# Optimization experiments

Measured on AMD Instinct MI355X. Metric: run time of the kernel, lower is better.

## Reference

```python
import jax, jax.numpy as jnp
import numpy as np

T, B, S, D = 128, 32, 100, 256  # targetL, batch, sourceL, output_size
EPS = 1e-6

def setup_inputs() -> dict:
    key = jax.random.key(0)
    ks = jax.random.split(key, 9)
    sc = 0.05  # weight init scale
    inp = {
        'prev_layer': jax.random.normal(ks[0], (T, B, D), dtype=jnp.float32),
        'hidden': jax.random.normal(ks[1], (B, D), dtype=jnp.float32),
        'enc_output': jax.random.normal(ks[2], (T * B, S, D), dtype=jnp.float32),
        # linear weights (layer_norm=True -> no biases on linears)
        'W_in': jax.random.normal(ks[3], (D, 3 * D), dtype=jnp.float32) * sc,
        'W_hid': jax.random.normal(ks[4], (D, D), dtype=jnp.float32) * sc,
        'W_ctx': jax.random.normal(ks[5], (D, D), dtype=jnp.float32) * sc,
        'W_enc': jax.random.normal(ks[6], (D, D), dtype=jnp.float32) * sc,
        'W_q': jax.random.normal(ks[7], (D, D), dtype=jnp.float32) * sc,   # MLPAttention query proj
        'v_att': jax.random.normal(ks[8], (D,), dtype=jnp.float32) * sc,  # MLPAttention score vector
        # layernorm affine params
        'g_pre': jnp.ones(3 * D, jnp.float32), 'b_pre': jnp.zeros(3 * D, jnp.float32),
        'g_enc': jnp.ones(D, jnp.float32), 'b_enc': jnp.zeros(D, jnp.float32),
        'g_h': jnp.ones(D, jnp.float32), 'b_h': jnp.zeros(D, jnp.float32),
        'g_c': jnp.ones(D, jnp.float32), 'b_c': jnp.zeros(D, jnp.float32),
        'g_q': jnp.ones(D, jnp.float32), 'b_q': jnp.zeros(D, jnp.float32),
    }
    return inp

def _ln(x, g, b):
    m = jnp.mean(x, axis=-1, keepdims=True)
    v = jnp.mean((x - m) ** 2, axis=-1, keepdims=True)
    return g * (x - m) / jnp.sqrt(v + EPS) + b

def reference(prev_layer, hidden, enc_output, W_in, W_hid, W_ctx, W_enc, W_q, v_att,
              g_pre, b_pre, g_enc, b_enc, g_h, b_h, g_c, b_c, g_q, b_q):
    Tl, Bb, Dd = prev_layer.shape
    # input / encoder projections (dropout=0 -> identity)
    preact = _ln(prev_layer @ W_in, g_pre, b_pre)        # [T,B,3D]
    pctx = _ln(enc_output @ W_enc, g_enc, b_enc)         # [T*B,S,D]
    z, h_gate, x_t = jnp.split(preact, 3, axis=-1)
    z = jax.nn.sigmoid(z)
    h_gate = jax.nn.sigmoid(h_gate)
    # SRU-style elementwise linear recurrence over time
    def step(h, zx):
        zt, xt = zx
        s = (1.0 - zt) * h + zt * xt
        return s, s
    final_h, ss = jax.lax.scan(step, hidden, (z, x_t))   # ss: [T,B,D]
    # MLP (Bahdanau) attention: scores = v . tanh(LN(Wq s) + pctx)
    q = _ln(ss @ W_q, g_q, b_q).reshape(Tl * Bb, 1, Dd)
    scores = jnp.einsum('nsd,d->ns', jnp.tanh(q + pctx), v_att)  # [T*B,S]
    attn = jax.nn.softmax(scores, axis=-1)
    attn_out = jnp.einsum('ns,nsd->nd', attn, pctx).reshape(Tl, Bb, Dd)
    attn_out = attn_out / np.sqrt(Dd).astype(np.float32)
    out = jnp.tanh(_ln(ss @ W_hid, g_h, b_h) + _ln(attn_out @ W_ctx, g_c, b_c))
    out = (1.0 - h_gate) * out + h_gate * prev_layer     # highway gate
    return out, final_h, attn
```

## Files before the change

### kernel.cpp

```cpp
#include <hip/hip_runtime.h>
#include <hip/hip_bf16.h>
#include <math.h>

typedef short  s16x8 __attribute__((ext_vector_type(8)));
typedef float  f32x4 __attribute__((ext_vector_type(4)));
typedef float  f32x2 __attribute__((ext_vector_type(2)));

#define LN_EPS 1e-6f

__device__ __forceinline__ unsigned short f2bf(float x) {
  union { float f; unsigned u; } v; v.f = x;
  unsigned r = v.u + 0x7FFFu + ((v.u >> 16) & 1u);
  return (unsigned short)(r >> 16);
}
__device__ __forceinline__ float bf2f(unsigned short u) {
  union { unsigned u; float f; } v; v.u = ((unsigned)u) << 16;
  return v.f;
}
__device__ __forceinline__ float bflo(unsigned u) {
  union { unsigned u; float f; } v; v.u = u << 16; return v.f;
}
__device__ __forceinline__ float bfhi(unsigned u) {
  union { unsigned u; float f; } v; v.u = u & 0xFFFF0000u; return v.f;
}
__device__ __forceinline__ unsigned pack_bf2(float a, float b) {
  __hip_bfloat162 h = __float22bfloat162_rn(make_float2(a, b));
  unsigned u; __builtin_memcpy(&u, &h, 4); return u;
}
__device__ __forceinline__ float fast_tanh(float x) {
  float e = __expf(2.0f * x);
  return 1.0f - 2.0f * __builtin_amdgcn_rcpf(e + 1.0f);
}
__device__ __forceinline__ float fast_sigmoid(float x) {
  return __builtin_amdgcn_rcpf(1.0f + __expf(-x));
}

template <int CTRL>
__device__ __forceinline__ float dpp_add(float v) {
  union { float f; int i; } a, r;
  a.f = v;
  r.i = __builtin_amdgcn_update_dpp(0, a.i, CTRL, 0xF, 0xF, true);
  return v + r.f;
}
template <int CTRL>
__device__ __forceinline__ float dpp_max(float v) {
  union { float f; int i; } a, r;
  a.f = v;
  r.i = __builtin_amdgcn_update_dpp(a.i, a.i, CTRL, 0xF, 0xF, false);
  return fmaxf(v, r.f);
}
__device__ __forceinline__ float bcast63(float v) {
  union { float f; int i; } a, r;
  a.f = v;
  r.i = __builtin_amdgcn_readlane(a.i, 63);
  return r.f;
}
__device__ __forceinline__ float wredsum(float v) {
  v = dpp_add<0x128>(v); v = dpp_add<0x124>(v); v = dpp_add<0x122>(v); v = dpp_add<0x121>(v);
  v = dpp_add<0x142>(v); v = dpp_add<0x143>(v);
  return bcast63(v);
}
__device__ __forceinline__ float wredmax(float v) {
  v = dpp_max<0x128>(v); v = dpp_max<0x124>(v); v = dpp_max<0x122>(v); v = dpp_max<0x121>(v);
  v = dpp_max<0x142>(v); v = dpp_max<0x143>(v);
  return bcast63(v);
}
__device__ __forceinline__ float red16(float v) {
  v = dpp_add<0x121>(v); v = dpp_add<0x122>(v); v = dpp_add<0x124>(v); v = dpp_add<0x128>(v);
  return v;
}

__device__ __forceinline__ f32x4 mfma16(s16x8 a, s16x8 b, f32x4 c) {
  return __builtin_amdgcn_mfma_f32_16x16x32_bf16(a, b, c, 0, 0, 0);
}

__device__ __forceinline__ void stage_rows(unsigned short* A, const float* src,
                                           int rows, int tid, int nthreads) {
  char* Ab = (char*)A;
  int nquads = rows * 64;
  #pragma unroll 4
  for (int p = tid; p < nquads; p += nthreads) {
    int row = p >> 6, kq = p & 63;
    f32x4 v = *(const f32x4*)(src + row * 256 + kq * 4);
    unsigned u0 = pack_bf2(v.x, v.y);
    unsigned u1 = pack_bf2(v.z, v.w);
    int byte = row * 512 + ((kq * 8) ^ ((row & 7) << 4));
    *(uint2*)(Ab + byte) = uint2{u0, u1};
  }
}

__device__ __forceinline__ s16x8 readA(const unsigned short* A, int row, int kk, int hi) {
  const char* Ab = (const char*)A;
  int byte = row * 512 + (((kk * 64) + hi * 16) ^ ((row & 7) << 4));
  return *(const s16x8*)(Ab + byte);
}
__device__ __forceinline__ s16x8 readB(const unsigned short* Bt, int col, int kk, int hi) {
  return *(const s16x8*)(Bt + col * 256 + kk * 32 + hi * 8);
}

__global__ __launch_bounds__(256) void k_convw(
    const float* Win, const float* Wq, const float* Whid, const float* Wctx, const float* Wenc,
    unsigned short* bt_in, unsigned short* bt_q, unsigned short* bt_hid,
    unsigned short* bt_ctx, unsigned short* bt_enc) {
  __shared__ unsigned short tile[32][34];
  int b = blockIdx.x;
  const float* src; unsigned short* dst; int N, tk, tn;
  if (b < 192) { src = Win; dst = bt_in; N = 768; tk = b & 7; tn = b >> 3; }
  else {
    int bb = b - 192; int m = bb >> 6; int r = bb & 63;
    tk = r & 7; tn = r >> 3; N = 256;
    src = (m == 0) ? Wq : (m == 1) ? Whid : (m == 2) ? Wctx : Wenc;
    dst = (m == 0) ? bt_q : (m == 1) ? bt_hid : (m == 2) ? bt_ctx : bt_enc;
  }
  int k0 = tk * 32, n0 = tn * 32;
  {
    int i = threadIdx.x >> 3, j4 = (threadIdx.x & 7) * 4;
    f32x4 v = *(const f32x4*)(src + (size_t)(k0 + i) * N + n0 + j4);
    *(unsigned*)((char*)&tile[i][j4])     = pack_bf2(v.x, v.y);
    *(unsigned*)((char*)&tile[i][j4 + 2]) = pack_bf2(v.z, v.w);
  }
  __syncthreads();
  {
    int j = threadIdx.x >> 3, i4 = (threadIdx.x & 7) * 4;
    unsigned lo = (unsigned)tile[i4 + 0][j] | ((unsigned)tile[i4 + 1][j] << 16);
    unsigned hi = (unsigned)tile[i4 + 2][j] | ((unsigned)tile[i4 + 3][j] << 16);
    *(uint2*)(dst + (size_t)(n0 + j) * 256 + k0 + i4) = uint2{lo, hi};
  }
}

__global__ __launch_bounds__(256) void k_preact(
    const float* prev, const unsigned short* bt_in,
    const float* g_pre, const float* b_pre,
    float* Z, float* HG, float* XT) {
  __shared__ __align__(16) unsigned short A[16 * 256];
  __shared__ float C[16 * 768];
  int tid = threadIdx.x, lane = tid & 63, wave = tid >> 6;
  int hi = lane >> 4, lo = lane & 15;
  int r0 = blockIdx.x * 16;
  stage_rows(A, prev + (size_t)r0 * 256, 16, tid, 256);
  __syncthreads();
  f32x4 acc[12];
  #pragma unroll
  for (int ct = 0; ct < 12; ct++) acc[ct] = f32x4{0.f, 0.f, 0.f, 0.f};
  #pragma unroll
  for (int kk = 0; kk < 8; kk++) {
    s16x8 a = readA(A, lo, kk, hi);
    #pragma unroll
    for (int ct = 0; ct < 12; ct++) {
      s16x8 b = readB(bt_in, wave * 192 + ct * 16 + lo, kk, hi);
      acc[ct] = mfma16(a, b, acc[ct]);
    }
  }
  #pragma unroll
  for (int ct = 0; ct < 12; ct++) {
    int col = wave * 192 + ct * 16 + lo;
    #pragma unroll
    for (int r = 0; r < 4; r++) C[(hi * 4 + r) * 768 + col] = acc[ct][r];
  }
  __syncthreads();
  #pragma unroll
  for (int mm = 0; mm < 4; mm++) {
    int m = wave * 4 + mm;
    float x[12]; float s = 0.f, q = 0.f;
    #pragma unroll
    for (int i = 0; i < 12; i++) {
      x[i] = C[m * 768 + lane + 64 * i];
      s += x[i]; q += x[i] * x[i];
    }
    s = wredsum(s); q = wredsum(q);
    float mean = s * (1.0f / 768.0f);
    float var = q * (1.0f / 768.0f) - mean * mean;
    float rstd = rsqrtf(var + LN_EPS);
    int gr = r0 + m;
    #pragma unroll
    for (int i = 0; i < 12; i++) {
      int c = lane + 64 * i;
      float y = g_pre[c] * (x[i] - mean) * rstd + b_pre[c];
      if (c < 256)      Z [gr * 256 + c]         = fast_sigmoid(y);
      else if (c < 512) HG[gr * 256 + (c - 256)] = fast_sigmoid(y);
      else              XT[gr * 256 + (c - 512)] = y;
    }
  }
}

__global__ __launch_bounds__(256) void k_scan(
    const float* hidden, const float* Z, const float* XT,
    float* SS, float* outFinalH) {
  int tid = blockIdx.x * 256 + threadIdx.x;
  float h = hidden[tid];
  for (int t0 = 0; t0 < 128; t0 += 8) {
    float zc[8], xc[8];
    #pragma unroll
    for (int j = 0; j < 8; j++) {
      zc[j] = Z [(t0 + j) * 8192 + tid];
      xc[j] = XT[(t0 + j) * 8192 + tid];
    }
    #pragma unroll
    for (int j = 0; j < 8; j++) {
      h = (1.0f - zc[j]) * h + zc[j] * xc[j];
      SS[(t0 + j) * 8192 + tid] = h;
    }
  }
  outFinalH[tid] = h;
}

__global__ __launch_bounds__(256) void k_qproj(
    const float* SS, const unsigned short* bt_q,
    const float* g_q, const float* b_q, float* Q) {
  __shared__ __align__(16) unsigned short A[16 * 256];
  __shared__ float C[16 * 256];
  int tid = threadIdx.x, lane = tid & 63, wave = tid >> 6;
  int hi = lane >> 4, lo = lane & 15;
  int r0 = blockIdx.x * 16;
  stage_rows(A, SS + (size_t)r0 * 256, 16, tid, 256);
  __syncthreads();
  f32x4 acc[4];
  #pragma unroll
  for (int ct = 0; ct < 4; ct++) acc[ct] = f32x4{0.f, 0.f, 0.f, 0.f};
  #pragma unroll
  for (int kk = 0; kk < 8; kk++) {
    s16x8 a = readA(A, lo, kk, hi);
    #pragma unroll
    for (int ct = 0; ct < 4; ct++) {
      s16x8 b = readB(bt_q, wave * 64 + ct * 16 + lo, kk, hi);
      acc[ct] = mfma16(a, b, acc[ct]);
    }
  }
  #pragma unroll
  for (int ct = 0; ct < 4; ct++) {
    int col = wave * 64 + ct * 16 + lo;
    #pragma unroll
    for (int r = 0; r < 4; r++) C[(hi * 4 + r) * 256 + col] = acc[ct][r];
  }
  __syncthreads();
  #pragma unroll
  for (int mm = 0; mm < 4; mm++) {
    int m = wave * 4 + mm;
    float x[4]; float s = 0.f, q = 0.f;
    #pragma unroll
    for (int i = 0; i < 4; i++) {
      x[i] = C[m * 256 + lane + 64 * i];
      s += x[i]; q += x[i] * x[i];
    }
    s = wredsum(s); q = wredsum(q);
    float mean = s * (1.0f / 256.0f);
    float var = q * (1.0f / 256.0f) - mean * mean;
    float rstd = rsqrtf(var + LN_EPS);
    int gr = r0 + m;
    #pragma unroll
    for (int i = 0; i < 4; i++) {
      int c = lane + 64 * i;
      Q[gr * 256 + c] = g_q[c] * (x[i] - mean) * rstd + b_q[c];
    }
  }
}

__global__ __launch_bounds__(1024, 8) void k_attn(
    const float* enc, const unsigned short* bt_enc, const float* Q,
    const float* g_enc, const float* b_enc, const float* v_att,
    float* AOUT, float* attnOut) {
  __shared__ __align__(16) unsigned short AP[112 * 256];
  __shared__ float statS[448];
  __shared__ float statQ[448];
  __shared__ float spart4[448];
  __shared__ __align__(16) float alpha[112];
  __shared__ __align__(8) f32x2 stats[112];
  __shared__ float beta_s;
  int n = blockIdx.x;
  int tid = threadIdx.x, lane = tid & 63, wave = tid >> 6;
  int hi = lane >> 4, lo = lane & 15;
  if (tid < 448) { statS[tid] = 0.f; statQ[tid] = 0.f; spart4[tid] = 0.f; }
  {
    const float* src = enc + (size_t)n * 25600;
    char* Ab = (char*)AP;
    #pragma unroll
    for (int i = 0; i < 6; i++) {
      int p = tid + i * 1024;
      int row = p >> 6, kq = p & 63;
      f32x4 v = *(const f32x4*)(src + row * 256 + kq * 4);
      int byte = row * 512 + ((kq * 8) ^ ((row & 7) << 4));
      *(uint2*)(Ab + byte) = uint2{pack_bf2(v.x, v.y), pack_bf2(v.z, v.w)};
    }
    if (tid < 256) {
      int p = 6144 + tid;
      int row = p >> 6, kq = p & 63;
      f32x4 v = *(const f32x4*)(src + row * 256 + kq * 4);
      int byte = row * 512 + ((kq * 8) ^ ((row & 7) << 4));
      *(uint2*)(Ab + byte) = uint2{pack_bf2(v.x, v.y), pack_bf2(v.z, v.w)};
    } else {
      int t = tid - 256;
      int row = 100 + (t >> 6), kq = t & 63;
      int byte = row * 512 + ((kq * 8) ^ ((row & 7) << 4));
      *(uint2*)(Ab + byte) = uint2{0u, 0u};
    }
  }
  __syncthreads();
  f32x4 acc[7];
  #pragma unroll
  for (int mt = 0; mt < 7; mt++) acc[mt] = f32x4{0.f, 0.f, 0.f, 0.f};
  #pragma unroll
  for (int kk = 0; kk < 8; kk++) {
    s16x8 b = readB(bt_enc, (wave << 4) + lo, kk, hi);
    #pragma unroll
    for (int mt = 0; mt < 7; mt++) {
      s16x8 a = readA(AP, mt * 16 + lo, kk, hi);
      acc[mt] = mfma16(a, b, acc[mt]);
    }
  }
  int bank = (wave & 3) * 112;
  #pragma unroll
  for (int mt = 0; mt < 7; mt++) {
    #pragma unroll
    for (int r = 0; r < 4; r++) {
      int row = mt * 16 + hi * 4 + r;
      float x = acc[mt][r];
      float s = red16(x);
      float q = red16(x * x);
      if (lo == 0 && row < 100) {
        atomicAdd(&statS[bank + row], s);
        atomicAdd(&statQ[bank + row], q);
      }
    }
  }
  __syncthreads();
  if (tid < 112) {
    float S  = (statS[tid] + statS[112 + tid]) + (statS[224 + tid] + statS[336 + tid]);
    float Qs = (statQ[tid] + statQ[112 + tid]) + (statQ[224 + tid] + statQ[336 + tid]);
    float mean = S * (1.0f / 256.0f);
    float var = Qs * (1.0f / 256.0f) - mean * mean;
    stats[tid] = f32x2{mean, rsqrtf(var + LN_EPS)};
  }
  __syncthreads();
  int c = (wave << 4) + lo;
  float gp = g_enc[c], bp = b_enc[c], vp = v_att[c], qp = Q[(size_t)n * 256 + c];
  #pragma unroll
  for (int mt = 0; mt < 7; mt++) {
    #pragma unroll
    for (int r = 0; r < 4; r++) {
      int row = mt * 16 + hi * 4 + r;
      f32x2 st = stats[row];
      float t = vp * fast_tanh(qp + fmaf(gp, (acc[mt][r] - st.x) * st.y, bp));
      t = red16(t);
      if (lo == 0 && row < 100) atomicAdd(&spart4[bank + row], t);
    }
  }
  __syncthreads();
  if (wave == 0) {
    int l2 = lane + 64;
    float s1 = (spart4[lane] + spart4[112 + lane]) + (spart4[224 + lane] + spart4[336 + lane]);
    float s2 = (lane < 36)
        ? (spart4[l2] + spart4[112 + l2]) + (spart4[224 + l2] + spart4[336 + l2])
        : -INFINITY;
    float mx = wredmax(fmaxf(s1, s2));
    float e1 = __expf(s1 - mx);
    float e2 = (lane < 36) ? __expf(s2 - mx) : 0.f;
    float sm = wredsum(e1 + e2);
    float inv = __builtin_amdgcn_rcpf(sm);
    float p1 = e1 * inv, p2 = e2 * inv;
    f32x2 st1 = stats[lane];
    float a1 = p1 * st1.y, bsum = a1 * st1.x;
    float a2 = 0.f;
    if (lane < 36) {
      f32x2 st2 = stats[l2];
      a2 = p2 * st2.y; bsum = fmaf(a2, st2.x, bsum);
    }
    alpha[lane] = a1;
    if (lane < 48) alpha[l2] = a2;
    float bp_ = wredsum(bsum);
    if (lane == 0) beta_s = bp_;
    attnOut[(size_t)n * 100 + lane] = p1;
    if (lane < 36) attnOut[(size_t)n * 100 + l2] = p2;
  }
  __syncthreads();
  float w = 0.f;
  #pragma unroll
  for (int mt = 0; mt < 7; mt++) {
    f32x4 al = *(const f32x4*)(alpha + mt * 16 + hi * 4);
    #pragma unroll
    for (int r = 0; r < 4; r++) w = fmaf(al[r], acc[mt][r], w);
  }
  w += __shfl_xor(w, 16); w += __shfl_xor(w, 32);
  if (lane < 16) {
    float y = fmaf(gp, w - beta_s, bp) * 0.0625f;
    AOUT[(size_t)n * 256 + c] = y;
  }
}

__global__ __launch_bounds__(256) void k_out(
    const float* SS, const float* AOUT,
    const unsigned short* bt_hid, const unsigned short* bt_ctx,
    const float* g_h, const float* b_h, const float* g_c, const float* b_c,
    const float* HG, const float* prev, float* out) {
  __shared__ __align__(16) unsigned short A1[16 * 256];
  __shared__ __align__(16) unsigned short A2[16 * 256];
  __shared__ float C1[16 * 256];
  __shared__ float C2[16 * 256];
  int tid = threadIdx.x, lane = tid & 63, wave = tid >> 6;
  int hi = lane >> 4, lo = lane & 15;
  int r0 = blockIdx.x * 16;
  stage_rows(A1, SS + (size_t)r0 * 256, 16, tid, 256);
  stage_rows(A2, AOUT + (size_t)r0 * 256, 16, tid, 256);
  __syncthreads();
  f32x4 acc1[4], acc2[4];
  #pragma unroll
  for (int ct = 0; ct < 4; ct++) {
    acc1[ct] = f32x4{0.f, 0.f, 0.f, 0.f};
    acc2[ct] = f32x4{0.f, 0.f, 0.f, 0.f};
  }
  #pragma unroll
  for (int kk = 0; kk < 8; kk++) {
    s16x8 a1 = readA(A1, lo, kk, hi);
    s16x8 a2 = readA(A2, lo, kk, hi);
    #pragma unroll
    for (int ct = 0; ct < 4; ct++) {
      int col = wave * 64 + ct * 16 + lo;
      s16x8 b1 = readB(bt_hid, col, kk, hi);
      s16x8 b2 = readB(bt_ctx, col, kk, hi);
      acc1[ct] = mfma16(a1, b1, acc1[ct]);
      acc2[ct] = mfma16(a2, b2, acc2[ct]);
    }
  }
  #pragma unroll
  for (int ct = 0; ct < 4; ct++) {
    int col = wave * 64 + ct * 16 + lo;
    #pragma unroll
    for (int r = 0; r < 4; r++) {
      C1[(hi * 4 + r) * 256 + col] = acc1[ct][r];
      C2[(hi * 4 + r) * 256 + col] = acc2[ct][r];
    }
  }
  __syncthreads();
  #pragma unroll
  for (int mm = 0; mm < 4; mm++) {
    int m = wave * 4 + mm;
    float x1[4], x2[4];
    float s1 = 0.f, q1 = 0.f, s2 = 0.f, q2 = 0.f;
    #pragma unroll
    for (int i = 0; i < 4; i++) {
      x1[i] = C1[m * 256 + lane + 64 * i];
      x2[i] = C2[m * 256 + lane + 64 * i];
      s1 += x1[i]; q1 += x1[i] * x1[i];
      s2 += x2[i]; q2 += x2[i] * x2[i];
    }
    s1 = wredsum(s1); q1 = wredsum(q1);
    s2 = wredsum(s2); q2 = wredsum(q2);
    float mean1 = s1 * (1.0f / 256.0f), var1 = q1 * (1.0f / 256.0f) - mean1 * mean1;
    float mean2 = s2 * (1.0f / 256.0f), var2 = q2 * (1.0f / 256.0f) - mean2 * mean2;
    float rstd1 = rsqrtf(var1 + LN_EPS), rstd2 = rsqrtf(var2 + LN_EPS);
    int gr = r0 + m;
    #pragma unroll
    for (int i = 0; i < 4; i++) {
      int cc = lane + 64 * i;
      float y1 = g_h[cc] * (x1[i] - mean1) * rstd1 + b_h[cc];
      float y2 = g_c[cc] * (x2[i] - mean2) * rstd2 + b_c[cc];
      float y = fast_tanh(y1 + y2);
      float g = HG[gr * 256 + cc];
      float pv = prev[gr * 256 + cc];
      out[gr * 256 + cc] = (1.0f - g) * y + g * pv;
    }
  }
}

extern "C" void kernel_launch(void* const* d_in, const int* in_sizes, int n_in,
                              void* d_out, int out_size, void* d_ws, size_t ws_size,
                              hipStream_t stream) {
  const float* prev   = (const float*)d_in[0];
  const float* hidden = (const float*)d_in[1];
  const float* enc    = (const float*)d_in[2];
  const float* W_in   = (const float*)d_in[3];
  const float* W_hid  = (const float*)d_in[4];
  const float* W_ctx  = (const float*)d_in[5];
  const float* W_enc  = (const float*)d_in[6];
  const float* W_q    = (const float*)d_in[7];
  const float* v_att  = (const float*)d_in[8];
  const float* g_pre  = (const float*)d_in[9];
  const float* b_pre  = (const float*)d_in[10];
  const float* g_enc  = (const float*)d_in[11];
  const float* b_enc  = (const float*)d_in[12];
  const float* g_h    = (const float*)d_in[13];
  const float* b_h    = (const float*)d_in[14];
  const float* g_c    = (const float*)d_in[15];
  const float* b_c    = (const float*)d_in[16];
  const float* g_q    = (const float*)d_in[17];
  const float* b_q    = (const float*)d_in[18];

  char* ws = (char*)d_ws;
  unsigned short* BT_IN  = (unsigned short*)(ws + 0);
  unsigned short* BT_Q   = (unsigned short*)(ws + 393216);
  unsigned short* BT_HID = (unsigned short*)(ws + 524288);
  unsigned short* BT_CTX = (unsigned short*)(ws + 655360);
  unsigned short* BT_ENC = (unsigned short*)(ws + 786432);
  float* Z    = (float*)(ws + 917504);
  float* HG   = (float*)(ws + 5111808);
  float* XT   = (float*)(ws + 9306112);
  float* SS   = (float*)(ws + 13500416);
  float* Q    = (float*)(ws + 17694720);
  float* AOUT = (float*)(ws + 21889024);

  float* out    = (float*)d_out;
  float* finalH = out + 1048576;
  float* attnO  = out + 1056768;

  k_convw <<<448, 256, 0, stream>>>(W_in, W_q, W_hid, W_ctx, W_enc,
                                    BT_IN, BT_Q, BT_HID, BT_CTX, BT_ENC);
  k_preact<<<256, 256, 0, stream>>>(prev, BT_IN, g_pre, b_pre, Z, HG, XT);
  k_scan  <<<32, 256, 0, stream>>>(hidden, Z, XT, SS, finalH);
  k_qproj <<<256, 256, 0, stream>>>(SS, BT_Q, g_q, b_q, Q);
  k_attn  <<<4096, 1024, 0, stream>>>(enc, BT_ENC, Q, g_enc, b_enc, v_att, AOUT, attnO);
  k_out   <<<256, 256, 0, stream>>>(SS, AOUT, BT_HID, BT_CTX,
                                    g_h, b_h, g_c, b_c, HG, prev, out);
}
```

Baseline: 272.7 us.

## Restructure attention kernel so each wave owns 16 source rows across all features

The attention kernel is changed from 16 waves that each own 16 feature columns across all rows to 7 waves that each own 16 source rows across all 256 features. The MFMA operands are swapped: encoder rows come from LDS, and the encoder weight is read straight from global memory. Because each row's full feature vector now sits in one wave, LayerNorm stats and tanh scores reduce with shuffles instead of shared-memory atomics, which removes two barriers and the atomic traffic. The cost is a larger accumulator set per thread (64 floats) and a cross-wave partial-sum pass through LDS for the weighted context.

```diff
diff --git a/kernel.cpp b/kernel.cpp
--- a/kernel.cpp
+++ b/kernel.cpp
@@ -16,12 +16,6 @@
 __device__ __forceinline__ float bf2f(unsigned short u) {
   union { unsigned u; float f; } v; v.u = ((unsigned)u) << 16;
   return v.f;
-}
-__device__ __forceinline__ float bflo(unsigned u) {
-  union { unsigned u; float f; } v; v.u = u << 16; return v.f;
-}
-__device__ __forceinline__ float bfhi(unsigned u) {
-  union { unsigned u; float f; } v; v.u = u & 0xFFFF0000u; return v.f;
 }
 __device__ __forceinline__ unsigned pack_bf2(float a, float b) {
   __hip_bfloat162 h = __float22bfloat162_rn(make_float2(a, b));
@@ -255,134 +249,121 @@
   }
 }
 
-__global__ __launch_bounds__(1024, 8) void k_attn(
+__global__ __launch_bounds__(448, 4) void k_attn(
     const float* enc, const unsigned short* bt_enc, const float* Q,
     const float* g_enc, const float* b_enc, const float* v_att,
     float* AOUT, float* attnOut) {
   __shared__ __align__(16) unsigned short AP[112 * 256];
-  __shared__ float statS[448];
-  __shared__ float statQ[448];
-  __shared__ float spart4[448];
-  __shared__ __align__(16) float alpha[112];
-  __shared__ __align__(8) f32x2 stats[112];
+  __shared__ __align__(16) f32x4 gbvq[256];
+  __shared__ float scoresL[112];
+  __shared__ float alpha[112];
   __shared__ float beta_s;
+  float* part = (float*)AP;
   int n = blockIdx.x;
   int tid = threadIdx.x, lane = tid & 63, wave = tid >> 6;
   int hi = lane >> 4, lo = lane & 15;
-  if (tid < 448) { statS[tid] = 0.f; statQ[tid] = 0.f; spart4[tid] = 0.f; }
-  {
-    const float* src = enc + (size_t)n * 25600;
-    char* Ab = (char*)AP;
-    #pragma unroll
-    for (int i = 0; i < 6; i++) {
-      int p = tid + i * 1024;
-      int row = p >> 6, kq = p & 63;
+  const float* src = enc + (size_t)n * 25600;
+  char* Ab = (char*)AP;
+  #pragma unroll
+  for (int i = 0; i < 14; i++) {
+    int p = tid + i * 448;
+    int row = p >> 6, kq = p & 63;
+    f32x4 v = *(const f32x4*)(src + row * 256 + kq * 4);
+    int byte = row * 512 + ((kq * 8) ^ ((row & 7) << 4));
+    *(uint2*)(Ab + byte) = uint2{pack_bf2(v.x, v.y), pack_bf2(v.z, v.w)};
+  }
+  #pragma unroll
+  for (int i = 14; i < 16; i++) {
+    int p = tid + i * 448;
+    int row = p >> 6, kq = p & 63;
+    uint2 u{0u, 0u};
+    if (row < 100) {
       f32x4 v = *(const f32x4*)(src + row * 256 + kq * 4);
-      int byte = row * 512 + ((kq * 8) ^ ((row & 7) << 4));
-      *(uint2*)(Ab + byte) = uint2{pack_bf2(v.x, v.y), pack_bf2(v.z, v.w)};
-    }
-    if (tid < 256) {
-      int p = 6144 + tid;
-      int row = p >> 6, kq = p & 63;
-      f32x4 v = *(const f32x4*)(src + row * 256 + kq * 4);
-      int byte = row * 512 + ((kq * 8) ^ ((row & 7) << 4));
-      *(uint2*)(Ab + byte) = uint2{pack_bf2(v.x, v.y), pack_bf2(v.z, v.w)};
-    } else {
-      int t = tid - 256;
-      int row = 100 + (t >> 6), kq = t & 63;
-      int byte = row * 512 + ((kq * 8) ^ ((row & 7) << 4));
-      *(uint2*)(Ab + byte) = uint2{0u, 0u};
-    }
-  }
-  __syncthreads();
-  f32x4 acc[7];
-  #pragma unroll
-  for (int mt = 0; mt < 7; mt++) acc[mt] = f32x4{0.f, 0.f, 0.f, 0.f};
+      u = uint2{pack_bf2(v.x, v.y), pack_bf2(v.z, v.w)};
+    }
+    int byte = row * 512 + ((kq * 8) ^ ((row & 7) << 4));
+    *(uint2*)(Ab + byte) = u;
+  }
+  if (tid < 256)
+    gbvq[tid] = f32x4{g_enc[tid], b_enc[tid], v_att[tid], Q[(size_t)n * 256 + tid]};
+  __syncthreads();
+  int sb = wave << 4;
+  f32x4 acc[16];
+  #pragma unroll
+  for (int mt = 0; mt < 16; mt++) acc[mt] = f32x4{0.f, 0.f, 0.f, 0.f};
   #pragma unroll
   for (int kk = 0; kk < 8; kk++) {
-    s16x8 b = readB(bt_enc, (wave << 4) + lo, kk, hi);
-    #pragma unroll
-    for (int mt = 0; mt < 7; mt++) {
-      s16x8 a = readA(AP, mt * 16 + lo, kk, hi);
+    s16x8 b = readA(AP, sb + lo, kk, hi);
+    const unsigned short* abase = bt_enc + lo * 256 + kk * 32 + hi * 8;
+    #pragma unroll
+    for (int mt = 0; mt < 16; mt++) {
+      s16x8 a = *(const s16x8*)(abase + mt * 4096);
       acc[mt] = mfma16(a, b, acc[mt]);
     }
   }
-  int bank = (wave & 3) * 112;
-  #pragma unroll
-  for (int mt = 0; mt < 7; mt++) {
+  float s1 = 0.f, s2 = 0.f;
+  #pragma unroll
+  for (int mt = 0; mt < 16; mt++) {
+    #pragma unroll
+    for (int r = 0; r < 4; r++) { float x = acc[mt][r]; s1 += x; s2 = fmaf(x, x, s2); }
+  }
+  s1 += __shfl_xor(s1, 16); s1 += __shfl_xor(s1, 32);
+  s2 += __shfl_xor(s2, 16); s2 += __shfl_xor(s2, 32);
+  float mean = s1 * (1.0f / 256.0f);
+  float var  = s2 * (1.0f / 256.0f) - mean * mean;
+  float rstd = rsqrtf(var + LN_EPS);
+  float c0f = fmaf(-mean, rstd, 0.f);
+  float sc = 0.f;
+  #pragma unroll
+  for (int mt = 0; mt < 16; mt++) {
     #pragma unroll
     for (int r = 0; r < 4; r++) {
-      int row = mt * 16 + hi * 4 + r;
-      float x = acc[mt][r];
-      float s = red16(x);
-      float q = red16(x * x);
-      if (lo == 0 && row < 100) {
-        atomicAdd(&statS[bank + row], s);
-        atomicAdd(&statQ[bank + row], q);
-      }
-    }
-  }
-  __syncthreads();
-  if (tid < 112) {
-    float S  = (statS[tid] + statS[112 + tid]) + (statS[224 + tid] + statS[336 + tid]);
-    float Qs = (statQ[tid] + statQ[112 + tid]) + (statQ[224 + tid] + statQ[336 + tid]);
-    float mean = S * (1.0f / 256.0f);
-    float var = Qs * (1.0f / 256.0f) - mean * mean;
-    stats[tid] = f32x2{mean, rsqrtf(var + LN_EPS)};
-  }
-  __syncthreads();
-  int c = (wave << 4) + lo;
-  float gp = g_enc[c], bp = b_enc[c], vp = v_att[c], qp = Q[(size_t)n * 256 + c];
-  #pragma unroll
-  for (int mt = 0; mt < 7; mt++) {
-    #pragma unroll
-    for (int r = 0; r < 4; r++) {
-      int row = mt * 16 + hi * 4 + r;
-      f32x2 st = stats[row];
-      float t = vp * fast_tanh(qp + fmaf(gp, (acc[mt][r] - st.x) * st.y, bp));
-      t = red16(t);
-      if (lo == 0 && row < 100) atomicAdd(&spart4[bank + row], t);
-    }
-  }
+      f32x4 t = gbvq[mt * 16 + (hi << 2) + r];
+      float ln = fmaf(acc[mt][r], rstd, c0f);
+      float arg = t.w + fmaf(t.x, ln, t.y);
+      sc = fmaf(t.z, fast_tanh(arg), sc);
+    }
+  }
+  sc += __shfl_xor(sc, 16); sc += __shfl_xor(sc, 32);
+  int s = sb + lo;
+  if (hi == 0 && s < 100) scoresL[s] = sc;
   __syncthreads();
   if (wave == 0) {
     int l2 = lane + 64;
-    float s1 = (spart4[lane] + spart4[112 + lane]) + (spart4[224 + lane] + spart4[336 + lane]);
-    float s2 = (lane < 36)
-        ? (spart4[l2] + spart4[112 + l2]) + (spart4[224 + l2] + spart4[336 + l2])
-        : -INFINITY;
-    float mx = wredmax(fmaxf(s1, s2));
-    float e1 = __expf(s1 - mx);
-    float e2 = (lane < 36) ? __expf(s2 - mx) : 0.f;
+    float a1s = scoresL[lane];
+    float a2s = (lane < 36) ? scoresL[l2] : -INFINITY;
+    float mx = wredmax(fmaxf(a1s, a2s));
+    float e1 = __expf(a1s - mx);
+    float e2 = (lane < 36) ? __expf(a2s - mx) : 0.f;
     float sm = wredsum(e1 + e2);
     float inv = __builtin_amdgcn_rcpf(sm);
     float p1 = e1 * inv, p2 = e2 * inv;
-    f32x2 st1 = stats[lane];
-    float a1 = p1 * st1.y, bsum = a1 * st1.x;
-    float a2 = 0.f;
-    if (lane < 36) {
-      f32x2 st2 = stats[l2];
-      a2 = p2 * st2.y; bsum = fmaf(a2, st2.x, bsum);
-    }
-    alpha[lane] = a1;
-    if (lane < 48) alpha[l2] = a2;
-    float bp_ = wredsum(bsum);
-    if (lane == 0) beta_s = bp_;
+    alpha[lane] = p1;
+    if (lane < 48) alpha[l2] = (lane < 36) ? p2 : 0.f;
+    if (lane == 0) beta_s = 0.f;
     attnOut[(size_t)n * 100 + lane] = p1;
     if (lane < 36) attnOut[(size_t)n * 100 + l2] = p2;
   }
   __syncthreads();
-  float w = 0.f;
-  #pragma unroll
-  for (int mt = 0; mt < 7; mt++) {
-    f32x4 al = *(const f32x4*)(alpha + mt * 16 + hi * 4);
-    #pragma unroll
-    for (int r = 0; r < 4; r++) w = fmaf(al[r], acc[mt][r], w);
-  }
-  w += __shfl_xor(w, 16); w += __shfl_xor(w, 32);
-  if (lane < 16) {
-    float y = fmaf(gp, w - beta_s, bp) * 0.0625f;
-    AOUT[(size_t)n * 256 + c] = y;
+  float p = alpha[sb + lo];
+  float al = p * rstd;
+  float bl = red16(al * mean);
+  if (lane == 0) atomicAdd(&beta_s, bl);
+  #pragma unroll
+  for (int mt = 0; mt < 16; mt++) {
+    #pragma unroll
+    for (int r = 0; r < 4; r++) {
+      float v = red16(al * acc[mt][r]);
+      if (lo == 0) part[wave * 256 + mt * 16 + (hi << 2) + r] = v;
+    }
+  }
+  __syncthreads();
+  if (tid < 256) {
+    float a = 0.f;
+    #pragma unroll
+    for (int w = 0; w < 7; w++) a += part[w * 256 + tid];
+    f32x4 t = gbvq[tid];
+    AOUT[(size_t)n * 256 + tid] = fmaf(t.x, a - beta_s, t.y) * 0.0625f;
   }
 }
 
@@ -506,7 +487,7 @@
   k_preact<<<256, 256, 0, stream>>>(prev, BT_IN, g_pre, b_pre, Z, HG, XT);
   k_scan  <<<32, 256, 0, stream>>>(hidden, Z, XT, SS, finalH);
   k_qproj <<<256, 256, 0, stream>>>(SS, BT_Q, g_q, b_q, Q);
-  k_attn  <<<4096, 1024, 0, stream>>>(enc, BT_ENC, Q, g_enc, b_enc, v_att, AOUT, attnO);
+  k_attn  <<<4096, 448, 0, stream>>>(enc, BT_ENC, Q, g_enc, b_enc, v_att, AOUT, attnO);
   k_out   <<<256, 256, 0, stream>>>(SS, AOUT, BT_HID, BT_CTX,
                                     g_h, b_h, g_c, b_c, HG, prev, out);
 }
```

Measured after the change: 614.6 us. 2.25x slower.
